# Performance work log

Measured on AMD Instinct MI355X. Metric: run time of the kernel, lower is better.

The kernel has to match this reference:

```python
import jax, jax.numpy as jnp
import numpy as np
from jax import lax

B, T, H_IN, W_IN = 16, 100, 159, 132   # T = n_frames (channels AND time steps)
HID = 100                               # lstm_h
NC, NL = 14, 3                          # num_classes, num_locations
FEAT = (H_IN - 27) * W_IN               # 17424, GRU input size


def setup_inputs() -> dict:
    key = jax.random.key(0)
    ks = jax.random.split(key, 16)
    s = 0.05
    return {
        "x":    jax.random.normal(ks[0], (B, T, H_IN, W_IN), jnp.float32),
        "w1":   jax.random.normal(ks[1], (T, T, 10, 1), jnp.float32) * s,
        "bc1":  jax.random.normal(ks[2], (T,), jnp.float32) * s,
        "w2":   jax.random.normal(ks[3], (T, T, 10, 1), jnp.float32) * s,
        "bc2":  jax.random.normal(ks[4], (T,), jnp.float32) * s,
        "w3":   jax.random.normal(ks[5], (T, T, 10, 1), jnp.float32) * s,
        "bc3":  jax.random.normal(ks[6], (T,), jnp.float32) * s,
        "w_ih": jax.random.normal(ks[7], (3 * HID, FEAT), jnp.float32) * 0.01,
        "w_hh": jax.random.normal(ks[8], (3 * HID, HID), jnp.float32) * s,
        "b_ih": jax.random.normal(ks[9], (3 * HID,), jnp.float32) * s,
        "b_hh": jax.random.normal(ks[10], (3 * HID,), jnp.float32) * s,
        "w_y1": jax.random.normal(ks[11], (NC, HID), jnp.float32) * s,
        "b_y1": jax.random.normal(ks[12], (NC,), jnp.float32) * s,
        "w_y2": jax.random.normal(ks[13], (NL, HID), jnp.float32) * s,
        "b_y2": jax.random.normal(ks[14], (NL,), jnp.float32) * s,
    }


def _conv(x, w, b):
    y = lax.conv_general_dilated(x, w, (1, 1), 'VALID',
                                 dimension_numbers=('NCHW', 'OIHW', 'NCHW'))
    return y + b[None, :, None, None]


def _gru(gi, w_ih, w_hh, b_ih, b_hh):
    # gi: [B, T, FEAT] batch_first; torch GRU gate order r, z, n
    xw = jnp.einsum('btf,gf->btg', gi, w_ih) + b_ih        # [B,T,3H]
    h0 = jnp.zeros((gi.shape[0], HID), gi.dtype)

    def step(h, xw_t):
        gh = h @ w_hh.T + b_hh                             # [B,3H]
        r = jax.nn.sigmoid(xw_t[:, :HID] + gh[:, :HID])
        z = jax.nn.sigmoid(xw_t[:, HID:2 * HID] + gh[:, HID:2 * HID])
        n = jnp.tanh(xw_t[:, 2 * HID:] + r * gh[:, 2 * HID:])
        h_new = (1.0 - z) * n + z * h
        return h_new, h_new

    _, hs = lax.scan(step, h0, jnp.swapaxes(xw, 0, 1))     # [T,B,H]
    return jnp.swapaxes(hs, 0, 1)                          # [B,T,H]


def reference(x, w1, bc1, w2, bc2, w3, bc3,
              w_ih, w_hh, b_ih, b_hh, w_y1, b_y1, w_y2, b_y2):
    c = _conv(_conv(_conv(x, w1, bc1), w2, bc2), w3, bc3)  # [B,T,H3,W]
    gi = c.reshape(c.shape[0], c.shape[1], -1)             # [B,T,FEAT]
    g = _gru(gi, w_ih, w_hh, b_ih, b_hh)                   # [B,T,HID]
    y1 = jax.nn.sigmoid(jnp.einsum('bth,ch->btc', g, w_y1) + b_y1)
    y2 = jnp.tanh(jnp.einsum('bth,ch->btc', g, w_y2) + b_y2) * 10.0
    return (y1, y2)
```

## Files before the change

kernel.cpp:

```cpp
#include <hip/hip_runtime.h>
#include <math.h>

#define TDIM  100
#define HIDN  100
#define G3    300
#define WD    132
#define CIP   104
#define KP    1056
#define NKC   33
#define GIK   17440
#define GIN   320
#define BTOT  16
#define INP0  (159 * WD)

typedef float    f32x4 __attribute__((ext_vector_type(4)));
typedef _Float16 f16x8 __attribute__((ext_vector_type(8)));
typedef _Float16 f16x4 __attribute__((ext_vector_type(4)));

static __device__ __forceinline__ float sigmoidf_(float x) {
    return 1.f / (1.f + __expf(-x));
}
static __device__ __forceinline__ float tanhf_(float x) {
    const float e = __expf(-2.f * fabsf(x));
    const float t = (1.f - e) / (1.f + e);
    return copysignf(t, x);
}
static __device__ __forceinline__ float bcastf(float v, int l) {
    return __int_as_float(__builtin_amdgcn_readlane(__float_as_int(v), l));
}

static __device__ __forceinline__ int xcd_remap_lin()
{
    const int nwg = gridDim.x * gridDim.y * gridDim.z;
    const int lin = (blockIdx.z * gridDim.y + blockIdx.y) * gridDim.x + blockIdx.x;
    const int q = nwg >> 3, r = nwg & 7;
    const int xcd = lin & 7, idx = lin >> 3;
    return (xcd < r ? xcd * (q + 1) : r * (q + 1) + (xcd - r) * q) + idx;
}

__global__ __launch_bounds__(256)
void prep_convw(const float* __restrict__ w, _Float16* __restrict__ wp)
{
    const int idx = blockIdx.x * 256 + threadIdx.x;
    if (idx >= 112 * KP) return;
    const int co = idx / KP, k = idx - co * KP;
    const int kh = k / CIP, ci = k - kh * CIP;
    float v = 0.f;
    if (co < 100 && ci < 100 && kh < 10)
        v = w[(co * 100 + ci) * 10 + kh];
    wp[idx] = (_Float16)v;
}

__global__ __launch_bounds__(256)
void prep_wih(const float* __restrict__ w_ih, _Float16* __restrict__ wihp)
{
    const int k = blockIdx.x * 256 + threadIdx.x;
    const int n = blockIdx.y;
    if (k >= GIK) return;
    const float v = (n < G3 && k < 17424) ? w_ih[(size_t)n * 17424 + k] : 0.f;
    wihp[(size_t)n * GIK + k] = (_Float16)v;
}

__global__ __launch_bounds__(256)
void transpose_x(const float* __restrict__ x, _Float16* __restrict__ xT)
{
    __shared__ __align__(16) _Float16 t[64][116];
    const int tid = threadIdx.x;
    const int p0  = blockIdx.x * 64;
    const int b   = blockIdx.y;
    const int pl  = tid & 63;
    const int p   = p0 + pl;
    t[tid >> 2][100 + (tid & 3)] = (_Float16)0.f;
    const float* xb = x + (size_t)b * 100 * INP0;
    #pragma unroll
    for (int i = 0; i < 25; ++i) {
        const int ci = (tid >> 6) + i * 4;
        const float v = (p < INP0) ? xb[(size_t)ci * INP0 + p] : 0.f;
        t[pl][ci] = (_Float16)v;
    }
    __syncthreads();
    _Float16* xTb = xT + (size_t)b * INP0 * CIP;
    #pragma unroll
    for (int i = 0; i < 7; ++i) {
        const int idx = tid + i * 256;
        if (idx < 64 * 26) {
            const int rr = idx / 26;
            const int c  = (idx - rr * 26) * 4;
            if (p0 + rr < INP0)
                *(f16x4*)(xTb + (size_t)(p0 + rr) * CIP + c) = *(const f16x4*)&t[rr][c];
        }
    }
}

template<int HIN, bool OUTT>
__global__ __launch_bounds__(256)
void conv_mfma(const _Float16* __restrict__ actT,
               const _Float16* __restrict__ wp,
               const float*    __restrict__ bias,
               _Float16* __restrict__ out)
{
    constexpr int HOUT = HIN - 9;
    constexpr int NP   = HOUT * WD;
    constexpr int INP  = HIN * WD;

    __shared__ __align__(16) _Float16 As[112][40];
    __shared__ __align__(16) _Float16 Bs[128][40];

    const int tid  = threadIdx.x;
    const int work = xcd_remap_lin();
    const int p0   = (work % gridDim.x) * 128;
    const int b    = work / gridDim.x;
    const _Float16* act_b = actT + (size_t)b * INP * CIP;

    f32x4 acc[7][2] = {};

    const int wv = tid >> 6;
    const int ln = tid & 15;
    const int lq = (tid & 63) >> 4;

    for (int kk = 0; kk < NKC; ++kk) {
        const int k0 = kk * 32;
        int idx = tid;
        #pragma unroll
        for (int i = 0; i < 2; ++i, idx += 256) {
            if (idx < 448) {
                const int co = idx >> 2, run = idx & 3;
                *(uint4*)&As[co][run * 8] =
                    *(const uint4*)(wp + co * KP + k0 + run * 8);
            }
        }
        idx = tid;
        #pragma unroll
        for (int i = 0; i < 2; ++i, idx += 256) {
            const int pl = idx >> 2, run = idx & 3;
            const int k  = k0 + run * 8;
            const int kh = k / CIP;
            const int ci0 = k - kh * CIP;
            int row = p0 + pl + kh * WD;
            row = min(row, INP - 1);
            *(uint4*)&Bs[pl][run * 8] =
                *(const uint4*)(act_b + (size_t)row * CIP + ci0);
        }
        __syncthreads();
        const f16x8 bf0 = *(const f16x8*)&Bs[(wv * 2 + 0) * 16 + ln][lq * 8];
        const f16x8 bf1 = *(const f16x8*)&Bs[(wv * 2 + 1) * 16 + ln][lq * 8];
        #pragma unroll
        for (int mt = 0; mt < 7; ++mt) {
            const f16x8 af = *(const f16x8*)&As[mt * 16 + ln][lq * 8];
            acc[mt][0] = __builtin_amdgcn_mfma_f32_16x16x32_f16(af, bf0, acc[mt][0], 0, 0, 0);
            acc[mt][1] = __builtin_amdgcn_mfma_f32_16x16x32_f16(af, bf1, acc[mt][1], 0, 0, 0);
        }
        __syncthreads();
    }

    #pragma unroll
    for (int j = 0; j < 2; ++j) {
        const int p = p0 + (wv * 2 + j) * 16 + ln;
        if (p >= NP) continue;
        if (OUTT) {
            _Float16* orow = out + (size_t)b * NP * CIP + (size_t)p * CIP;
            #pragma unroll
            for (int mt = 0; mt < 7; ++mt) {
                const int co0 = mt * 16 + lq * 4;
                if (co0 < CIP) {
                    f16x4 v;
                    #pragma unroll
                    for (int r = 0; r < 4; ++r) {
                        const int co = co0 + r;
                        v[r] = (_Float16)(acc[mt][j][r] + (co < 100 ? bias[co] : 0.f));
                    }
                    *(f16x4*)(orow + co0) = v;
                }
            }
        } else {
            #pragma unroll
            for (int mt = 0; mt < 7; ++mt) {
                #pragma unroll
                for (int r = 0; r < 4; ++r) {
                    const int co = mt * 16 + lq * 4 + r;
                    if (co < 100)
                        out[((size_t)b * 100 + co) * GIK + p] =
                            (_Float16)(acc[mt][j][r] + bias[co]);
                }
            }
        }
    }
}

__global__ __launch_bounds__(256)
void gemm_mfma(const _Float16* __restrict__ A,
               const _Float16* __restrict__ B,
               float* __restrict__ C)
{
    constexpr int NKG = GIK / 32;
    constexpr int SEG = 69;
    __shared__ __align__(16) _Float16 As[64][40];
    __shared__ __align__(16) _Float16 Bs[64][40];

    const int tid  = threadIdx.x;
    const int work = xcd_remap_lin();
    const int bx   = work % 5;
    const int rem  = work / 5;
    const int by   = rem % 25;
    const int bz   = rem / 25;

    const int n0  = bx * 64;
    const int m0  = by * 64;
    const int k00 = bz * SEG;
    const int k01 = min(NKG, k00 + SEG);

    const int wv = tid >> 6, ln = tid & 15, lq = (tid & 63) >> 4;
    const int r = tid >> 2, run = tid & 3;

    f32x4 acc[4] = {};

    for (int kk = k00; kk < k01; ++kk) {
        const int k0 = kk * 32;
        *(uint4*)&As[r][run * 8] = *(const uint4*)(A + (size_t)(m0 + r) * GIK + k0 + run * 8);
        *(uint4*)&Bs[r][run * 8] = *(const uint4*)(B + (size_t)(n0 + r) * GIK + k0 + run * 8);
        __syncthreads();
        const f16x8 af = *(const f16x8*)&As[wv * 16 + ln][lq * 8];
        #pragma unroll
        for (int nt = 0; nt < 4; ++nt) {
            const f16x8 bf = *(const f16x8*)&Bs[nt * 16 + ln][lq * 8];
            acc[nt] = __builtin_amdgcn_mfma_f32_16x16x32_f16(af, bf, acc[nt], 0, 0, 0);
        }
        __syncthreads();
    }
    #pragma unroll
    for (int nt = 0; nt < 4; ++nt) {
        const int n = n0 + nt * 16 + ln;
        if (n < G3) {
            const int m = m0 + wv * 16 + lq * 4;
            #pragma unroll
            for (int rr = 0; rr < 4; ++rr)
                atomicAdd(&C[(size_t)(m + rr) * G3 + n], acc[nt][rr]);
        }
    }
}

__global__ __launch_bounds__(256)
void init_xw_k(const float* __restrict__ b_ih, float* __restrict__ xw)
{
    const int i = blockIdx.x * 256 + threadIdx.x;
    if (i < BTOT * TDIM * G3) xw[i] = b_ih[i % G3];
}

__global__ __launch_bounds__(640)
void gru3_k(const float* __restrict__ xw, const float* __restrict__ w_hh,
            const float* __restrict__ b_hh, float* __restrict__ gout)
{
    __shared__ float h_s[128];
    __shared__ float ghp[2][304];

    const int tid  = threadIdx.x;
    const int b    = blockIdx.x;
    const int wave = tid >> 6;
    const int lane = tid & 63;
    const int half = (wave >= 5) ? 1 : 0;
    const int row  = (half ? wave - 5 : wave) * 64 + lane;
    const bool act = (row < G3);

    float wreg[50];
    #pragma unroll
    for (int j = 0; j < 50; ++j)
        wreg[j] = act ? w_hh[row * HIDN + half * 50 + j] : 0.f;
    const float bh = (act && half == 0) ? b_hh[row] : 0.f;

    if (tid < 128) h_s[tid] = 0.f;
    __syncthreads();

    const bool gate = (tid < HIDN);
    const float* xwb = xw + (size_t)b * TDIM * G3;

    float xA0 = 0.f, xA1 = 0.f, xA2 = 0.f;
    float xB0 = 0.f, xB1 = 0.f, xB2 = 0.f;
    if (gate) {
        xA0 = xwb[tid];
        xA1 = xwb[HIDN + tid];
        xA2 = xwb[2 * HIDN + tid];
    }

    auto matvec = [&]() {
        const float hlo = h_s[lane];
        const float hhi = h_s[64 + lane];
        float acc = bh;
        if (half == 0) {
            #pragma unroll
            for (int k = 0; k < 50; ++k)
                acc += wreg[k] * bcastf(hlo, k);
        } else {
            #pragma unroll
            for (int k = 0; k < 14; ++k)
                acc += wreg[k] * bcastf(hlo, 50 + k);
            #pragma unroll
            for (int k = 14; k < 50; ++k)
                acc += wreg[k] * bcastf(hhi, k - 14);
        }
        if (act) ghp[half][row] = acc;
    };

    auto gates = [&](int t, float x0, float x1, float x2) {
        if (gate) {
            const float g0 = ghp[0][tid]            + ghp[1][tid];
            const float g1 = ghp[0][HIDN + tid]     + ghp[1][HIDN + tid];
            const float g2 = ghp[0][2 * HIDN + tid] + ghp[1][2 * HIDN + tid];
            const float hp = h_s[tid];
            const float r  = sigmoidf_(x0 + g0);
            const float z  = sigmoidf_(x1 + g1);
            const float n  = tanhf_(x2 + r * g2);
            const float hn = (1.f - z) * n + z * hp;
            h_s[tid] = hn;
            gout[((size_t)b * TDIM + t) * HIDN + tid] = hn;
        }
    };

    for (int t = 0; t < TDIM; t += 2) {
        if (gate && t + 1 < TDIM) {
            const float* p = xwb + (size_t)(t + 1) * G3;
            xB0 = p[tid]; xB1 = p[HIDN + tid]; xB2 = p[2 * HIDN + tid];
        }
        matvec();
        __syncthreads();
        gates(t, xA0, xA1, xA2);
        __syncthreads();

        if (gate && t + 2 < TDIM) {
            const float* p = xwb + (size_t)(t + 2) * G3;
            xA0 = p[tid]; xA1 = p[HIDN + tid]; xA2 = p[2 * HIDN + tid];
        }
        matvec();
        __syncthreads();
        gates(t + 1, xB0, xB1, xB2);
        __syncthreads();
    }
}

__global__ __launch_bounds__(256)
void heads_k(const float* __restrict__ g,
             const float* __restrict__ wy1, const float* __restrict__ by1,
             const float* __restrict__ wy2, const float* __restrict__ by2,
             float* __restrict__ out)
{
    constexpr int NY1 = BTOT * TDIM * 14;
    constexpr int NY2 = BTOT * TDIM * 3;
    const int idx = blockIdx.x * 256 + threadIdx.x;
    if (idx < NY1) {
        const int row = idx / 14, c = idx - row * 14;
        const float* gr = g + (size_t)row * HIDN;
        const float* wr = wy1 + c * HIDN;
        float acc = by1[c];
        for (int k = 0; k < HIDN; ++k) acc += gr[k] * wr[k];
        out[idx] = sigmoidf_(acc);
    } else if (idx < NY1 + NY2) {
        const int j = idx - NY1;
        const int row = j / 3, c = j - row * 3;
        const float* gr = g + (size_t)row * HIDN;
        const float* wr = wy2 + c * HIDN;
        float acc = by2[c];
        for (int k = 0; k < HIDN; ++k) acc += gr[k] * wr[k];
        out[NY1 + row * 3 + c] = tanhf(acc) * 10.f;
    }
}

extern "C" void kernel_launch(void* const* d_in, const int* in_sizes, int n_in,
                              void* d_out, int out_size, void* d_ws, size_t ws_size,
                              hipStream_t stream)
{
    (void)in_sizes; (void)n_in; (void)out_size; (void)ws_size;
    const float* x    = (const float*)d_in[0];
    const float* w1   = (const float*)d_in[1];
    const float* bc1  = (const float*)d_in[2];
    const float* w2   = (const float*)d_in[3];
    const float* bc2  = (const float*)d_in[4];
    const float* w3   = (const float*)d_in[5];
    const float* bc3  = (const float*)d_in[6];
    const float* w_ih = (const float*)d_in[7];
    const float* w_hh = (const float*)d_in[8];
    const float* b_ih = (const float*)d_in[9];
    const float* b_hh = (const float*)d_in[10];
    const float* wy1  = (const float*)d_in[11];
    const float* by1  = (const float*)d_in[12];
    const float* wy2  = (const float*)d_in[13];
    const float* by2  = (const float*)d_in[14];
    float* out = (float*)d_out;

    char* wsp = (char*)d_ws;
    auto alloc = [&](size_t bytes) -> char* {
        char* p = wsp; wsp += (bytes + 255) & ~(size_t)255; return p;
    };
    _Float16* wp1  = (_Float16*)alloc((size_t)112 * KP * 2);
    _Float16* wp2  = (_Float16*)alloc((size_t)112 * KP * 2);
    _Float16* wp3  = (_Float16*)alloc((size_t)112 * KP * 2);
    float*    xw   = (float*)   alloc((size_t)BTOT * TDIM * G3 * 4);
    float*    g    = (float*)   alloc((size_t)BTOT * TDIM * HIDN * 4);
    char*     regA = alloc((size_t)BTOT * INP0 * CIP * 2);
    char*     regB = alloc((size_t)BTOT * 150 * WD * CIP * 2);

    _Float16* xT   = (_Float16*)regA;
    _Float16* c2T  = (_Float16*)regA;
    _Float16* wihp = (_Float16*)regA;
    _Float16* c1T  = (_Float16*)regB;
    _Float16* gi   = (_Float16*)regB;

    prep_convw<<<(112 * KP + 255) / 256, 256, 0, stream>>>(w1, wp1);
    prep_convw<<<(112 * KP + 255) / 256, 256, 0, stream>>>(w2, wp2);
    prep_convw<<<(112 * KP + 255) / 256, 256, 0, stream>>>(w3, wp3);
    init_xw_k<<<(BTOT * TDIM * G3 + 255) / 256, 256, 0, stream>>>(b_ih, xw);

    transpose_x<<<dim3((INP0 + 63) / 64, BTOT), 256, 0, stream>>>(x, xT);
    conv_mfma<159, true ><<<dim3(155, BTOT), 256, 0, stream>>>(xT,  wp1, bc1, c1T);
    conv_mfma<150, true ><<<dim3(146, BTOT), 256, 0, stream>>>(c1T, wp2, bc2, c2T);
    conv_mfma<141, false><<<dim3(137, BTOT), 256, 0, stream>>>(c2T, wp3, bc3, gi);

    prep_wih<<<dim3((GIK + 255) / 256, GIN), 256, 0, stream>>>(w_ih, wihp);
    gemm_mfma<<<dim3(5, 25, 8), 256, 0, stream>>>(gi, wihp, xw);
    gru3_k<<<16, 640, 0, stream>>>(xw, w_hh, b_hh, g);
    heads_k<<<(27200 + 255) / 256, 256, 0, stream>>>(g, wy1, by1, wy2, by2, out);
}
```

Before: 995.5 us.

## Double-buffer conv and GEMM tiles with direct global-to-LDS async loads

The conv and GRU input-projection GEMM kernels now use two LDS buffers per operand and fill them with global_load_lds 16-byte transfers. The next K-chunk is prefetched while MFMAs run on the current one, and the two __syncthreads per iteration become explicit vmcnt/lgkmcnt waits plus barriers. The goal is to hide global load latency and drop the register round trip for staging. The LDS rows lose their padding (stride 32 instead of 40), which may add bank conflicts. The packed conv weights are padded to 128 rows so every wave loads uniformly.

```diff
diff --git a/kernel.cpp b/kernel.cpp
--- a/kernel.cpp
+++ b/kernel.cpp
@@ -29,6 +29,14 @@
     return __int_as_float(__builtin_amdgcn_readlane(__float_as_int(v), l));
 }
 
+static __device__ __forceinline__ void gl16(const _Float16* g, _Float16* l)
+{
+    __builtin_amdgcn_global_load_lds(
+        (const __attribute__((address_space(1))) void*)g,
+        (__attribute__((address_space(3))) void*)l,
+        16, 0, 0);
+}
+
 static __device__ __forceinline__ int xcd_remap_lin()
 {
     const int nwg = gridDim.x * gridDim.y * gridDim.z;
@@ -42,7 +50,7 @@
 void prep_convw(const float* __restrict__ w, _Float16* __restrict__ wp)
 {
     const int idx = blockIdx.x * 256 + threadIdx.x;
-    if (idx >= 112 * KP) return;
+    if (idx >= 128 * KP) return;
     const int co = idx / KP, k = idx - co * KP;
     const int kh = k / CIP, ci = k - kh * CIP;
     float v = 0.f;
@@ -103,8 +111,8 @@
     constexpr int NP   = HOUT * WD;
     constexpr int INP  = HIN * WD;
 
-    __shared__ __align__(16) _Float16 As[112][40];
-    __shared__ __align__(16) _Float16 Bs[128][40];
+    __shared__ __align__(16) _Float16 As[2][128][32];
+    __shared__ __align__(16) _Float16 Bs[2][128][32];
 
     const int tid  = threadIdx.x;
     const int work = xcd_remap_lin();
@@ -112,45 +120,52 @@
     const int b    = work / gridDim.x;
     const _Float16* act_b = actT + (size_t)b * INP * CIP;
 
-    f32x4 acc[7][2] = {};
-
     const int wv = tid >> 6;
+    const int l  = tid & 63;
     const int ln = tid & 15;
     const int lq = (tid & 63) >> 4;
-
+    const int rl  = l >> 2;
+    const int run = l & 3;
+
+    const _Float16* srcA0 = wp + (size_t)(wv * 16 + rl) * KP + run * 8;
+    const _Float16* srcA1 = wp + (size_t)(64 + wv * 16 + rl) * KP + run * 8;
+    const int plB0 = wv * 32 + rl;
+    const int plB1 = wv * 32 + 16 + rl;
+
+    f32x4 acc[7][2] = {};
+
+    auto stage = [&](int buf, int kk) {
+        const int k0 = kk * 32;
+        gl16(srcA0 + k0, &As[buf][wv * 16][0]);
+        gl16(srcA1 + k0, &As[buf][64 + wv * 16][0]);
+        const int k   = k0 + run * 8;
+        const int kh  = k / CIP;
+        const int ci0 = k - kh * CIP;
+        const int row0 = min(p0 + plB0 + kh * WD, INP - 1);
+        const int row1 = min(p0 + plB1 + kh * WD, INP - 1);
+        gl16(act_b + (size_t)row0 * CIP + ci0, &Bs[buf][wv * 32][0]);
+        gl16(act_b + (size_t)row1 * CIP + ci0, &Bs[buf][wv * 32 + 16][0]);
+    };
+
+    stage(0, 0);
+    int cur = 0;
     for (int kk = 0; kk < NKC; ++kk) {
-        const int k0 = kk * 32;
-        int idx = tid;
-        #pragma unroll
-        for (int i = 0; i < 2; ++i, idx += 256) {
-            if (idx < 448) {
-                const int co = idx >> 2, run = idx & 3;
-                *(uint4*)&As[co][run * 8] =
-                    *(const uint4*)(wp + co * KP + k0 + run * 8);
-            }
-        }
-        idx = tid;
-        #pragma unroll
-        for (int i = 0; i < 2; ++i, idx += 256) {
-            const int pl = idx >> 2, run = idx & 3;
-            const int k  = k0 + run * 8;
-            const int kh = k / CIP;
-            const int ci0 = k - kh * CIP;
-            int row = p0 + pl + kh * WD;
-            row = min(row, INP - 1);
-            *(uint4*)&Bs[pl][run * 8] =
-                *(const uint4*)(act_b + (size_t)row * CIP + ci0);
-        }
-        __syncthreads();
-        const f16x8 bf0 = *(const f16x8*)&Bs[(wv * 2 + 0) * 16 + ln][lq * 8];
-        const f16x8 bf1 = *(const f16x8*)&Bs[(wv * 2 + 1) * 16 + ln][lq * 8];
+        if (kk + 1 < NKC) {
+            stage(cur ^ 1, kk + 1);
+            asm volatile("s_waitcnt vmcnt(4)\n\ts_barrier" ::: "memory");
+        } else {
+            asm volatile("s_waitcnt vmcnt(0)\n\ts_barrier" ::: "memory");
+        }
+        const f16x8 bf0 = *(const f16x8*)&Bs[cur][(wv * 2 + 0) * 16 + ln][lq * 8];
+        const f16x8 bf1 = *(const f16x8*)&Bs[cur][(wv * 2 + 1) * 16 + ln][lq * 8];
         #pragma unroll
         for (int mt = 0; mt < 7; ++mt) {
-            const f16x8 af = *(const f16x8*)&As[mt * 16 + ln][lq * 8];
+            const f16x8 af = *(const f16x8*)&As[cur][mt * 16 + ln][lq * 8];
             acc[mt][0] = __builtin_amdgcn_mfma_f32_16x16x32_f16(af, bf0, acc[mt][0], 0, 0, 0);
             acc[mt][1] = __builtin_amdgcn_mfma_f32_16x16x32_f16(af, bf1, acc[mt][1], 0, 0, 0);
         }
-        __syncthreads();
+        asm volatile("s_waitcnt lgkmcnt(0)\n\ts_barrier" ::: "memory");
+        cur ^= 1;
     }
 
     #pragma unroll
@@ -194,8 +209,8 @@
 {
     constexpr int NKG = GIK / 32;
     constexpr int SEG = 69;
-    __shared__ __align__(16) _Float16 As[64][40];
-    __shared__ __align__(16) _Float16 Bs[64][40];
+    __shared__ __align__(16) _Float16 As[2][64][32];
+    __shared__ __align__(16) _Float16 Bs[2][64][32];
 
     const int tid  = threadIdx.x;
     const int work = xcd_remap_lin();
@@ -210,22 +225,37 @@
     const int k01 = min(NKG, k00 + SEG);
 
     const int wv = tid >> 6, ln = tid & 15, lq = (tid & 63) >> 4;
-    const int r = tid >> 2, run = tid & 3;
+    const int l  = tid & 63;
+    const int rl = l >> 2, run = l & 3;
+
+    const _Float16* srcA = A + (size_t)(m0 + wv * 16 + rl) * GIK + run * 8;
+    const _Float16* srcB = B + (size_t)(n0 + wv * 16 + rl) * GIK + run * 8;
 
     f32x4 acc[4] = {};
 
+    auto stage = [&](int buf, int kk) {
+        const int k0 = kk * 32;
+        gl16(srcA + k0, &As[buf][wv * 16][0]);
+        gl16(srcB + k0, &Bs[buf][wv * 16][0]);
+    };
+
+    stage(0, k00);
+    int cur = 0;
     for (int kk = k00; kk < k01; ++kk) {
-        const int k0 = kk * 32;
-        *(uint4*)&As[r][run * 8] = *(const uint4*)(A + (size_t)(m0 + r) * GIK + k0 + run * 8);
-        *(uint4*)&Bs[r][run * 8] = *(const uint4*)(B + (size_t)(n0 + r) * GIK + k0 + run * 8);
-        __syncthreads();
-        const f16x8 af = *(const f16x8*)&As[wv * 16 + ln][lq * 8];
+        if (kk + 1 < k01) {
+            stage(cur ^ 1, kk + 1);
+            asm volatile("s_waitcnt vmcnt(2)\n\ts_barrier" ::: "memory");
+        } else {
+            asm volatile("s_waitcnt vmcnt(0)\n\ts_barrier" ::: "memory");
+        }
+        const f16x8 af = *(const f16x8*)&As[cur][wv * 16 + ln][lq * 8];
         #pragma unroll
         for (int nt = 0; nt < 4; ++nt) {
-            const f16x8 bf = *(const f16x8*)&Bs[nt * 16 + ln][lq * 8];
+            const f16x8 bf = *(const f16x8*)&Bs[cur][nt * 16 + ln][lq * 8];
             acc[nt] = __builtin_amdgcn_mfma_f32_16x16x32_f16(af, bf, acc[nt], 0, 0, 0);
         }
-        __syncthreads();
+        asm volatile("s_waitcnt lgkmcnt(0)\n\ts_barrier" ::: "memory");
+        cur ^= 1;
     }
     #pragma unroll
     for (int nt = 0; nt < 4; ++nt) {
@@ -389,9 +419,9 @@
     auto alloc = [&](size_t bytes) -> char* {
         char* p = wsp; wsp += (bytes + 255) & ~(size_t)255; return p;
     };
-    _Float16* wp1  = (_Float16*)alloc((size_t)112 * KP * 2);
-    _Float16* wp2  = (_Float16*)alloc((size_t)112 * KP * 2);
-    _Float16* wp3  = (_Float16*)alloc((size_t)112 * KP * 2);
+    _Float16* wp1  = (_Float16*)alloc((size_t)128 * KP * 2);
+    _Float16* wp2  = (_Float16*)alloc((size_t)128 * KP * 2);
+    _Float16* wp3  = (_Float16*)alloc((size_t)128 * KP * 2);
     float*    xw   = (float*)   alloc((size_t)BTOT * TDIM * G3 * 4);
     float*    g    = (float*)   alloc((size_t)BTOT * TDIM * HIDN * 4);
     char*     regA = alloc((size_t)BTOT * INP0 * CIP * 2);
@@ -403,9 +433,9 @@
     _Float16* c1T  = (_Float16*)regB;
     _Float16* gi   = (_Float16*)regB;
 
-    prep_convw<<<(112 * KP + 255) / 256, 256, 0, stream>>>(w1, wp1);
-    prep_convw<<<(112 * KP + 255) / 256, 256, 0, stream>>>(w2, wp2);
-    prep_convw<<<(112 * KP + 255) / 256, 256, 0, stream>>>(w3, wp3);
+    prep_convw<<<(128 * KP + 255) / 256, 256, 0, stream>>>(w1, wp1);
+    prep_convw<<<(128 * KP + 255) / 256, 256, 0, stream>>>(w2, wp2);
+    prep_convw<<<(128 * KP + 255) / 256, 256, 0, stream>>>(w3, wp3);
     init_xw_k<<<(BTOT * TDIM * G3 + 255) / 256, 256, 0, stream>>>(b_ih, xw);
 
     transpose_x<<<dim3((INP0 + 63) / 64, BTOT), 256, 0, stream>>>(x, xT);
```

Measured after the change: 847.4 us. 1.17x faster.
